# Optimization experiments

Measured on AMD Instinct MI355X. Metric: run time of the kernel, lower is better.

## Reference

```python
import jax, jax.numpy as jnp
import numpy as np

G, H = 8, 512           # num_blocks, model_dim
L, C, A = 32, 32, 4     # latent_size, latent_categories_size, action_size
I = L * C + A           # GRU input size = 1028
B, T = 128, 64          # batch, seq_len


def setup_inputs() -> dict:
    key = jax.random.key(0)
    kz, ka, kwi, kwh, kbi, kbh = jax.random.split(key, 6)
    s = 1.0 / np.sqrt(H)  # PyTorch GRU default init scale
    return {
        "z": jax.random.normal(kz, (B, T, L * C), dtype=jnp.float32),
        "a": jax.random.normal(ka, (B, T, A), dtype=jnp.float32),
        "h": jnp.zeros((B, G * H), dtype=jnp.float32),
        "W_ih": jax.random.uniform(kwi, (G, 3 * H, I), jnp.float32, -s, s),
        "W_hh": jax.random.uniform(kwh, (G, 3 * H, H), jnp.float32, -s, s),
        "b_ih": jax.random.uniform(kbi, (G, 3 * H), jnp.float32, -s, s),
        "b_hh": jax.random.uniform(kbh, (G, 3 * H), jnp.float32, -s, s),
    }


def reference(z, a, h, W_ih, W_hh, b_ih, b_hh):
    b, t = z.shape[0], z.shape[1]
    x = jnp.concatenate([a, z], axis=-1)                    # (B,T,I)
    h0 = h.reshape(b, G, H)                                 # (B,G,H) block states
    # Precompute all input projections for every block/gate at once.
    x_proj = jnp.einsum('bti,gji->btgj', x, W_ih) + b_ih    # (B,T,G,3H)

    def step(hc, xp):  # hc: (B,G,H), xp: (B,G,3H)
        hp = jnp.einsum('bgh,gjh->bgj', hc, W_hh) + b_hh    # (B,G,3H)
        xr, xz, xn = jnp.split(xp, 3, axis=-1)
        hr, hz, hn = jnp.split(hp, 3, axis=-1)
        r = jax.nn.sigmoid(xr + hr)
        u = jax.nn.sigmoid(xz + hz)
        n = jnp.tanh(xn + r * hn)
        h_new = (1.0 - u) * n + u * hc
        return h_new, h_new

    _, ys = jax.lax.scan(step, h0, jnp.moveaxis(x_proj, 1, 0))  # ys: (T,B,G,H)
    out = jnp.moveaxis(ys, 0, 1).reshape(b, t, G * H)           # concat blocks on last dim
    return out
```

## Files before the change

### kernel.cpp

```cpp
#include <hip/hip_runtime.h>
#include <stdint.h>

#define G 8
#define H 512
#define I_RAW 1028
#define I_PAD 1056
#define BB 128
#define TT 64
#define GH (G*H)
#define G3H (G*3*H)
#define M_TOT (BB*TT)
#define N3H (3*H)

typedef __attribute__((ext_vector_type(8))) short bf16x8;
typedef __attribute__((ext_vector_type(4))) float f32x4;

__device__ __forceinline__ unsigned short f2bf(float f) {
  unsigned int u = __float_as_uint(f);
  u += 0x7fffu + ((u >> 16) & 1u);
  return (unsigned short)(u >> 16);
}
__device__ __forceinline__ float bf2f(unsigned short h) {
  return __uint_as_float(((unsigned int)h) << 16);
}

__global__ void k_pack_x(const float* __restrict__ z, const float* __restrict__ a,
                         unsigned short* __restrict__ xb) {
  int idx = blockIdx.x * 256 + threadIdx.x;
  if (idx >= M_TOT * I_PAD) return;
  int m = idx / I_PAD, i = idx % I_PAD;
  int b = m >> 6, t = m & 63;
  float v = 0.f;
  if (i < 4)            v = a[((size_t)b * TT + t) * 4 + i];
  else if (i < I_RAW)   v = z[((size_t)b * TT + t) * 1024 + (i - 4)];
  xb[idx] = f2bf(v);
}

__global__ void k_pack_wih(const float* __restrict__ w, unsigned short* __restrict__ wb) {
  int idx = blockIdx.x * 256 + threadIdx.x;
  if (idx >= G * N3H * I_PAD) return;
  int gj = idx / I_PAD, i = idx % I_PAD;
  float v = (i < I_RAW) ? w[(size_t)gj * I_RAW + i] : 0.f;
  wb[idx] = f2bf(v);
}

__global__ void k_pack_whh(const float* __restrict__ w, unsigned short* __restrict__ wb) {
  int idx = blockIdx.x * 256 + threadIdx.x;
  if (idx >= G * N3H * H) return;
  wb[idx] = f2bf(w[idx]);
}

__global__ void k_init_h(const float* __restrict__ h, unsigned short* __restrict__ hb0,
                         int* __restrict__ barcnt) {
  int idx = blockIdx.x * 256 + threadIdx.x;
  if (idx < 8 * 16) barcnt[idx] = 0;
  if (idx >= BB * GH) return;
  hb0[idx] = f2bf(h[idx]);
}

#define LROW 80

__launch_bounds__(256, 2)
__global__ void k_xproj(const unsigned short* __restrict__ xb,
                        const unsigned short* __restrict__ wihb,
                        unsigned short* __restrict__ xp,
                        int t0, int tcShift) {
  __shared__ char lA[128 * LROW];
  __shared__ char lB[128 * LROW];
  int blk = blockIdx.x;
  int by = blk / (G3H / 128);
  int bx = blk % (G3H / 128);
  int m0 = by * 128, n0 = bx * 128;
  int tid = threadIdx.x;
  int lane = tid & 63, wave = tid >> 6;
  int wm = (wave >> 1) * 64, wn = (wave & 1) * 64;
  int tcMask = (1 << tcShift) - 1;

  f32x4 acc[4][4] = {};

  for (int kt = 0; kt < I_PAD / 32; ++kt) {
    int k0 = kt * 32;
#pragma unroll
    for (int p = 0; p < 2; ++p) {
      int row = p * 64 + (tid >> 2);
      int c = (tid & 3) * 16;
      int rc = m0 + row;
      int b = rc >> tcShift, tl = rc & tcMask;
      const char* srcA = (const char*)&xb[(size_t)(b * TT + t0 + tl) * I_PAD + k0] + c;
      *(uint4*)(lA + row * LROW + c) = *(const uint4*)srcA;
      const char* srcB = (const char*)&wihb[(size_t)(n0 + row) * I_PAD + k0] + c;
      *(uint4*)(lB + row * LROW + c) = *(const uint4*)srcB;
    }
    __syncthreads();

    bf16x8 af[4], bf[4];
#pragma unroll
    for (int mt = 0; mt < 4; ++mt) {
      int r = wm + mt * 16 + (lane & 15);
      af[mt] = *(const bf16x8*)(lA + r * LROW + ((lane >> 4) * 16));
    }
#pragma unroll
    for (int nt = 0; nt < 4; ++nt) {
      int r = wn + nt * 16 + (lane & 15);
      bf[nt] = *(const bf16x8*)(lB + r * LROW + ((lane >> 4) * 16));
    }
#pragma unroll
    for (int mt = 0; mt < 4; ++mt)
#pragma unroll
      for (int nt = 0; nt < 4; ++nt)
        acc[mt][nt] = __builtin_amdgcn_mfma_f32_16x16x32_bf16(af[mt], bf[nt], acc[mt][nt], 0, 0, 0);
    __syncthreads();
  }

#pragma unroll
  for (int mt = 0; mt < 4; ++mt)
#pragma unroll
    for (int nt = 0; nt < 4; ++nt)
#pragma unroll
      for (int j = 0; j < 4; ++j) {
        int m = m0 + wm + mt * 16 + (lane >> 4) * 4 + j;
        int n = n0 + wn + nt * 16 + (lane & 15);
        xp[(size_t)m * G3H + n] = f2bf(acc[mt][nt][j]);
      }
}

__launch_bounds__(512, 2)
__global__ void k_scan(const unsigned short* __restrict__ xp,
                       const unsigned short* __restrict__ whhb,
                       const float* __restrict__ b_ih,
                       const float* __restrict__ b_hh,
                       const float* __restrict__ hsrc, int hstride,
                       unsigned short* __restrict__ hbuf0,
                       unsigned short* __restrict__ hbuf1,
                       float* __restrict__ out,
                       int* __restrict__ barcnt,
                       int t0, int Tc, int tcShift) {
  __shared__ char wlds[48 * 1024];
  int blk = blockIdx.x;
  int g = blk & 7;
  int i0 = (blk >> 3) << 4;
  int tid = threadIdx.x, lane = tid & 63, wave = tid >> 6;
  const unsigned short* wg_w = whhb + (size_t)g * N3H * H;

  for (int s = tid; s < 3072; s += 512) {
    int q = s >> 10, kt = (s >> 6) & 15, l = s & 63;
    int j = q * H + i0 + (l & 15);
    int k = kt * 32 + (l >> 4) * 8;
    *(bf16x8*)(wlds + (size_t)s * 16) = *(const bf16x8*)&wg_w[(size_t)j * H + k];
  }

  int ic = lane & 15;
  int i = i0 + ic;
  float brc = b_ih[g * N3H + 0 * H + i] + b_hh[g * N3H + 0 * H + i];
  float bzc = b_ih[g * N3H + 1 * H + i] + b_hh[g * N3H + 1 * H + i];
  float bin = b_ih[g * N3H + 2 * H + i];
  float bhn = b_hh[g * N3H + 2 * H + i];

  float hprev[4];
#pragma unroll
  for (int j = 0; j < 4; ++j) {
    int b = wave * 16 + (lane >> 4) * 4 + j;
    hprev[j] = hsrc[(size_t)b * hstride + g * H + i];
  }

  int arow = wave * 16 + (lane & 15);
  int akoff = (lane >> 4) * 8;
  int* cnt = &barcnt[g * 16];

  __syncthreads();

  for (int tl = 0; tl < Tc; ++tl) {
    int t = t0 + tl;
    const unsigned short* hin = (t & 1) ? hbuf1 : hbuf0;
    unsigned short* hout = (t & 1) ? hbuf0 : hbuf1;

    bf16x8 af[16];
#pragma unroll
    for (int kt = 0; kt < 16; ++kt)
      af[kt] = *(const bf16x8*)&hin[(size_t)arow * GH + g * H + kt * 32 + akoff];

    f32x4 acc[3] = {};
#pragma unroll
    for (int kt = 0; kt < 16; ++kt) {
#pragma unroll
      for (int q = 0; q < 3; ++q) {
        bf16x8 wf = *(const bf16x8*)(wlds + ((size_t)(q * 16 + kt) * 64 + lane) * 16);
        acc[q] = __builtin_amdgcn_mfma_f32_16x16x32_bf16(af[kt], wf, acc[q], 0, 0, 0);
      }
    }

#pragma unroll
    for (int j = 0; j < 4; ++j) {
      int b = wave * 16 + (lane >> 4) * 4 + j;
      size_t xrow = ((size_t)((b << tcShift) + tl)) * G3H + (size_t)g * N3H;
      float xr = bf2f(xp[xrow + 0 * H + i]);
      float xz = bf2f(xp[xrow + 1 * H + i]);
      float xn = bf2f(xp[xrow + 2 * H + i]);
      float r = 1.f / (1.f + __expf(-(xr + acc[0][j] + brc)));
      float u = 1.f / (1.f + __expf(-(xz + acc[1][j] + bzc)));
      float nn = xn + bin + r * (acc[2][j] + bhn);
      float th = 1.f - 2.f / (1.f + __expf(2.f * nn));
      float hnew = (1.f - u) * th + u * hprev[j];
      hprev[j] = hnew;
      hout[(size_t)b * GH + g * H + i] = f2bf(hnew);
      out[((size_t)b * TT + t) * GH + g * H + i] = hnew;
    }

    asm volatile("s_waitcnt vmcnt(0)" ::: "memory");
    __syncthreads();
    if (tid == 0) {
      __hip_atomic_fetch_add(cnt, 1, __ATOMIC_RELAXED, __HIP_MEMORY_SCOPE_AGENT);
      if (tl != Tc - 1) {
        int target = 32 * (t + 1);
        while (__hip_atomic_load(cnt, __ATOMIC_ACQUIRE, __HIP_MEMORY_SCOPE_AGENT) < target)
          __builtin_amdgcn_s_sleep(1);
      }
    }
    __syncthreads();
  }
}

extern "C" void kernel_launch(void* const* d_in, const int* in_sizes, int n_in,
                              void* d_out, int out_size, void* d_ws, size_t ws_size,
                              hipStream_t stream) {
  const float* z    = (const float*)d_in[0];
  const float* a    = (const float*)d_in[1];
  const float* h0   = (const float*)d_in[2];
  const float* Wih  = (const float*)d_in[3];
  const float* Whh  = (const float*)d_in[4];
  const float* bih  = (const float*)d_in[5];
  const float* bhh  = (const float*)d_in[6];
  float* out = (float*)d_out;

  char* ws = (char*)d_ws;
  const size_t XB_OFF  = 0;
  const size_t WIH_OFF = XB_OFF  + (size_t)M_TOT * I_PAD * 2;
  const size_t WHH_OFF = WIH_OFF + (size_t)G * N3H * I_PAD * 2;
  const size_t HB_OFF  = WHH_OFF + (size_t)G * N3H * H * 2;
  const size_t BAR_OFF = HB_OFF  + 2 * (size_t)BB * GH * 2;
  const size_t XP_OFF  = BAR_OFF + 512;
  const size_t FIXED   = XP_OFF;

  const size_t XP_ROW = (size_t)BB * G3H * 2;
  int tcShift = 6;
  while (tcShift > 0 && FIXED + (XP_ROW << tcShift) > ws_size) --tcShift;
  const int Tc = 1 << tcShift;

  unsigned short* xb   = (unsigned short*)(ws + XB_OFF);
  unsigned short* wihb = (unsigned short*)(ws + WIH_OFF);
  unsigned short* whhb = (unsigned short*)(ws + WHH_OFF);
  unsigned short* hb   = (unsigned short*)(ws + HB_OFF);
  int*            barcnt = (int*)(ws + BAR_OFF);
  unsigned short* xp   = (unsigned short*)(ws + XP_OFF);

  unsigned short* hbuf0 = hb;
  unsigned short* hbuf1 = hb + (size_t)BB * GH;

  {
    int n = M_TOT * I_PAD;
    k_pack_x<<<(n + 255) / 256, 256, 0, stream>>>(z, a, xb);
  }
  {
    int n = G * N3H * I_PAD;
    k_pack_wih<<<(n + 255) / 256, 256, 0, stream>>>(Wih, wihb);
  }
  {
    int n = G * N3H * H;
    k_pack_whh<<<(n + 255) / 256, 256, 0, stream>>>(Whh, whhb);
  }
  {
    int n = BB * GH;
    k_init_h<<<(n + 255) / 256, 256, 0, stream>>>(h0, hbuf0, barcnt);
  }

  for (int t0 = 0; t0 < TT; t0 += Tc) {
    int mtiles = (BB * Tc) / 128;
    k_xproj<<<mtiles * (G3H / 128), 256, 0, stream>>>(xb, wihb, xp, t0, tcShift);

    const float* hsrc = (t0 == 0) ? h0 : (const float*)(out + (size_t)(t0 - 1) * GH);
    int hstride = (t0 == 0) ? GH : TT * GH;
    int t0v = t0, tcv = Tc, tsv = tcShift;
    void* args[] = { (void*)&xp, (void*)&whhb, (void*)&bih, (void*)&bhh,
                     (void*)&hsrc, (void*)&hstride, (void*)&hbuf0, (void*)&hbuf1,
                     (void*)&out, (void*)&barcnt, (void*)&t0v, (void*)&tcv, (void*)&tsv };
    hipLaunchCooperativeKernel((void*)k_scan, dim3(256), dim3(512), args, 0, stream);
  }
}
```

Before: 997.0 us.

## Repack input projections for vector loads and overlap output stores with barrier

The input-projection GEMM now writes its results in a time-major layout. The r/z/n gate values for four batch rows sit next to each other, so each scan thread can fetch them with three 8-byte loads instead of twelve scattered 2-byte loads. Each step prefetches the next step's projections and moves the fp32 output stores to after the barrier arrive, before the spin-wait, so both overlap the grid-wide synchronisation. Barrier counters are spaced further apart to avoid sharing cache lines. The risk is extra register use, and outstanding stores and loads may delay the next step's waitcnt.

```diff
diff --git a/kernel.cpp b/kernel.cpp
--- a/kernel.cpp
+++ b/kernel.cpp
@@ -14,6 +14,7 @@
 
 typedef __attribute__((ext_vector_type(8))) short bf16x8;
 typedef __attribute__((ext_vector_type(4))) float f32x4;
+typedef __attribute__((ext_vector_type(4))) unsigned short u16x4;
 
 __device__ __forceinline__ unsigned short f2bf(float f) {
   unsigned int u = __float_as_uint(f);
@@ -53,7 +54,7 @@
 __global__ void k_init_h(const float* __restrict__ h, unsigned short* __restrict__ hb0,
                          int* __restrict__ barcnt) {
   int idx = blockIdx.x * 256 + threadIdx.x;
-  if (idx < 8 * 16) barcnt[idx] = 0;
+  if (idx < 8 * 32) barcnt[idx] = 0;
   if (idx >= BB * GH) return;
   hb0[idx] = f2bf(h[idx]);
 }
@@ -63,8 +64,8 @@
 __launch_bounds__(256, 2)
 __global__ void k_xproj(const unsigned short* __restrict__ xb,
                         const unsigned short* __restrict__ wihb,
-                        unsigned short* __restrict__ xp,
-                        int t0, int tcShift) {
+                        unsigned short* __restrict__ xp3,
+                        int t0) {
   __shared__ char lA[128 * LROW];
   __shared__ char lB[128 * LROW];
   int blk = blockIdx.x;
@@ -74,7 +75,6 @@
   int tid = threadIdx.x;
   int lane = tid & 63, wave = tid >> 6;
   int wm = (wave >> 1) * 64, wn = (wave & 1) * 64;
-  int tcMask = (1 << tcShift) - 1;
 
   f32x4 acc[4][4] = {};
 
@@ -85,7 +85,7 @@
       int row = p * 64 + (tid >> 2);
       int c = (tid & 3) * 16;
       int rc = m0 + row;
-      int b = rc >> tcShift, tl = rc & tcMask;
+      int b = rc & (BB - 1), tl = rc >> 7;
       const char* srcA = (const char*)&xb[(size_t)(b * TT + t0 + tl) * I_PAD + k0] + c;
       *(uint4*)(lA + row * LROW + c) = *(const uint4*)srcA;
       const char* srcB = (const char*)&wihb[(size_t)(n0 + row) * I_PAD + k0] + c;
@@ -115,17 +115,27 @@
 #pragma unroll
   for (int mt = 0; mt < 4; ++mt)
 #pragma unroll
-    for (int nt = 0; nt < 4; ++nt)
-#pragma unroll
-      for (int j = 0; j < 4; ++j) {
-        int m = m0 + wm + mt * 16 + (lane >> 4) * 4 + j;
-        int n = n0 + wn + nt * 16 + (lane & 15);
-        xp[(size_t)m * G3H + n] = f2bf(acc[mt][nt][j]);
-      }
+    for (int nt = 0; nt < 4; ++nt) {
+      int m = m0 + wm + mt * 16 + (lane >> 4) * 4;
+      int tl = m >> 7;
+      int bq = (m & (BB - 1)) >> 2;
+      int n = n0 + wn + nt * 16 + (lane & 15);
+      int g = n / N3H;
+      int rem = n - g * N3H;
+      int q = rem >> 9;
+      int i = rem & (H - 1);
+      u16x4 v;
+      v[0] = f2bf(acc[mt][nt][0]);
+      v[1] = f2bf(acc[mt][nt][1]);
+      v[2] = f2bf(acc[mt][nt][2]);
+      v[3] = f2bf(acc[mt][nt][3]);
+      size_t addr = ((((size_t)tl * (BB / 4) + bq) * G + g) * H + i) * 16 + q * 4;
+      *(u16x4*)&xp3[addr] = v;
+    }
 }
 
 __launch_bounds__(512, 2)
-__global__ void k_scan(const unsigned short* __restrict__ xp,
+__global__ void k_scan(const unsigned short* __restrict__ xp3,
                        const unsigned short* __restrict__ whhb,
                        const float* __restrict__ b_ih,
                        const float* __restrict__ b_hh,
@@ -134,7 +144,7 @@
                        unsigned short* __restrict__ hbuf1,
                        float* __restrict__ out,
                        int* __restrict__ barcnt,
-                       int t0, int Tc, int tcShift) {
+                       int t0, int Tc) {
   __shared__ char wlds[48 * 1024];
   int blk = blockIdx.x;
   int g = blk & 7;
@@ -165,9 +175,17 @@
 
   int arow = wave * 16 + (lane & 15);
   int akoff = (lane >> 4) * 8;
-  int* cnt = &barcnt[g * 16];
+  int* cnt = &barcnt[g * 32];
+
+  int bq = wave * 4 + (lane >> 4);
+  const unsigned short* xbase = xp3 + ((((size_t)bq) * G + g) * H + i) * 16;
+  const size_t xstep = (size_t)(BB / 4) * G * H * 16;
 
   __syncthreads();
+
+  u16x4 xq[3];
+#pragma unroll
+  for (int q = 0; q < 3; ++q) xq[q] = *(const u16x4*)(xbase + q * 4);
 
   for (int tl = 0; tl < Tc; ++tl) {
     int t = t0 + tl;
@@ -189,32 +207,43 @@
       }
     }
 
+    float hn4[4];
 #pragma unroll
     for (int j = 0; j < 4; ++j) {
       int b = wave * 16 + (lane >> 4) * 4 + j;
-      size_t xrow = ((size_t)((b << tcShift) + tl)) * G3H + (size_t)g * N3H;
-      float xr = bf2f(xp[xrow + 0 * H + i]);
-      float xz = bf2f(xp[xrow + 1 * H + i]);
-      float xn = bf2f(xp[xrow + 2 * H + i]);
+      float xr = bf2f(xq[0][j]);
+      float xz = bf2f(xq[1][j]);
+      float xn = bf2f(xq[2][j]);
       float r = 1.f / (1.f + __expf(-(xr + acc[0][j] + brc)));
       float u = 1.f / (1.f + __expf(-(xz + acc[1][j] + bzc)));
       float nn = xn + bin + r * (acc[2][j] + bhn);
       float th = 1.f - 2.f / (1.f + __expf(2.f * nn));
       float hnew = (1.f - u) * th + u * hprev[j];
       hprev[j] = hnew;
+      hn4[j] = hnew;
       hout[(size_t)b * GH + g * H + i] = f2bf(hnew);
-      out[((size_t)b * TT + t) * GH + g * H + i] = hnew;
     }
 
     asm volatile("s_waitcnt vmcnt(0)" ::: "memory");
     __syncthreads();
-    if (tid == 0) {
+    if (tid == 0)
       __hip_atomic_fetch_add(cnt, 1, __ATOMIC_RELAXED, __HIP_MEMORY_SCOPE_AGENT);
-      if (tl != Tc - 1) {
-        int target = 32 * (t + 1);
-        while (__hip_atomic_load(cnt, __ATOMIC_ACQUIRE, __HIP_MEMORY_SCOPE_AGENT) < target)
-          __builtin_amdgcn_s_sleep(1);
-      }
+
+#pragma unroll
+    for (int j = 0; j < 4; ++j) {
+      int b = wave * 16 + (lane >> 4) * 4 + j;
+      out[((size_t)b * TT + t) * GH + g * H + i] = hn4[j];
+    }
+    if (tl + 1 < Tc) {
+      const unsigned short* xb2 = xbase + (size_t)(tl + 1) * xstep;
+#pragma unroll
+      for (int q = 0; q < 3; ++q) xq[q] = *(const u16x4*)(xb2 + q * 4);
+    }
+
+    if (tid == 0 && tl != Tc - 1) {
+      int target = 32 * (t + 1);
+      while (__hip_atomic_load(cnt, __ATOMIC_ACQUIRE, __HIP_MEMORY_SCOPE_AGENT) < target)
+        __builtin_amdgcn_s_sleep(1);
     }
     __syncthreads();
   }
@@ -238,10 +267,10 @@
   const size_t WHH_OFF = WIH_OFF + (size_t)G * N3H * I_PAD * 2;
   const size_t HB_OFF  = WHH_OFF + (size_t)G * N3H * H * 2;
   const size_t BAR_OFF = HB_OFF  + 2 * (size_t)BB * GH * 2;
-  const size_t XP_OFF  = BAR_OFF + 512;
+  const size_t XP_OFF  = BAR_OFF + 1024;
   const size_t FIXED   = XP_OFF;
 
-  const size_t XP_ROW = (size_t)BB * G3H * 2;
+  const size_t XP_ROW = (size_t)(BB / 4) * G * H * 16 * 2;
   int tcShift = 6;
   while (tcShift > 0 && FIXED + (XP_ROW << tcShift) > ws_size) --tcShift;
   const int Tc = 1 << tcShift;
@@ -251,7 +280,7 @@
   unsigned short* whhb = (unsigned short*)(ws + WHH_OFF);
   unsigned short* hb   = (unsigned short*)(ws + HB_OFF);
   int*            barcnt = (int*)(ws + BAR_OFF);
-  unsigned short* xp   = (unsigned short*)(ws + XP_OFF);
+  unsigned short* xp3  = (unsigned short*)(ws + XP_OFF);
 
   unsigned short* hbuf0 = hb;
   unsigned short* hbuf1 = hb + (size_t)BB * GH;
@@ -274,15 +303,14 @@
   }
 
   for (int t0 = 0; t0 < TT; t0 += Tc) {
-    int mtiles = (BB * Tc) / 128;
-    k_xproj<<<mtiles * (G3H / 128), 256, 0, stream>>>(xb, wihb, xp, t0, tcShift);
+    k_xproj<<<Tc * (G3H / 128), 256, 0, stream>>>(xb, wihb, xp3, t0);
 
     const float* hsrc = (t0 == 0) ? h0 : (const float*)(out + (size_t)(t0 - 1) * GH);
     int hstride = (t0 == 0) ? GH : TT * GH;
-    int t0v = t0, tcv = Tc, tsv = tcShift;
-    void* args[] = { (void*)&xp, (void*)&whhb, (void*)&bih, (void*)&bhh,
+    int t0v = t0, tcv = Tc;
+    void* args[] = { (void*)&xp3, (void*)&whhb, (void*)&bih, (void*)&bhh,
                      (void*)&hsrc, (void*)&hstride, (void*)&hbuf0, (void*)&hbuf1,
-                     (void*)&out, (void*)&barcnt, (void*)&t0v, (void*)&tcv, (void*)&tsv };
+                     (void*)&out, (void*)&barcnt, (void*)&t0v, (void*)&tcv };
     hipLaunchCooperativeKernel((void*)k_scan, dim3(256), dim3(512), args, 0, stream);
   }
 }
```

Measured after the change: 1.015 ms. About the same (+1.9%).
